# Optimization experiments

Measured on AMD Instinct MI355X. Metric: run time of the kernel, lower is better.

Reference implementation:

```python
import jax, jax.numpy as jnp
import numpy as np

B, L, D = 8, 4096, 1024


def setup_inputs() -> dict:
    key = jax.random.key(0)
    k1, k2, k3 = jax.random.split(key, 3)
    x = jax.random.normal(k1, (B, L, D), dtype=jnp.float32)
    # nn.Linear(d_model, d_model): weight [D, D] (out, in), bias [D]
    bound = 1.0 / np.sqrt(D)
    W = jax.random.uniform(k2, (D, D), dtype=jnp.float32, minval=-bound, maxval=bound)
    b = jax.random.uniform(k3, (D,), dtype=jnp.float32, minval=-bound, maxval=bound)
    return {"x": x, "W": W, "b": b}


def reference(x, W, b):
    # rfft then irfft with n = original length along the sequence dim.
    # (Mathematically the identity on real input, but we keep the ops to
    # match the original module's computation faithfully.)
    x_fft = jnp.fft.rfft(x, axis=1)                 # [B, L//2+1, D] complex64
    x_ifft = jnp.fft.irfft(x_fft, n=x.shape[1], axis=1)  # [B, L, D] float32
    # nn.Linear: y = x @ W^T + b
    return jnp.einsum('bld,ed->ble', x_ifft, W) + b
```

## Files before the change

kernel.cpp:

```cpp
#include <hip/hip_runtime.h>
#include <hip/hip_bf16.h>
#include <stdint.h>


typedef __bf16 bf16_t;
typedef __bf16 bf16x8 __attribute__((ext_vector_type(8)));
typedef float f32x4 __attribute__((ext_vector_type(4)));

typedef __attribute__((address_space(1))) const void gvoid;
typedef __attribute__((address_space(3))) void svoid;

__global__ __launch_bounds__(256) void cvt_f32_bf16_kernel(const float* __restrict__ in,
                                                           bf16_t* __restrict__ out, int n8) {
  int i = blockIdx.x * 256 + threadIdx.x;
  if (i >= n8) return;
  const f32x4* p = (const f32x4*)in + (size_t)i * 2;
  f32x4 v0 = p[0];
  f32x4 v1 = p[1];
  bf16x8 o;
  o[0] = (bf16_t)v0[0]; o[1] = (bf16_t)v0[1]; o[2] = (bf16_t)v0[2]; o[3] = (bf16_t)v0[3];
  o[4] = (bf16_t)v1[0]; o[5] = (bf16_t)v1[1]; o[6] = (bf16_t)v1[2]; o[7] = (bf16_t)v1[3];
  *(bf16x8*)(out + (size_t)i * 8) = o;
}

__global__ __launch_bounds__(256) void gemm_bt_bias_kernel(
    const bf16_t* __restrict__ A, const bf16_t* __restrict__ B,
    const float* __restrict__ bias, float* __restrict__ C,
    int M, int N, int K) {
  __shared__ __align__(16) bf16_t As[128 * 32];
  __shared__ __align__(16) bf16_t Bs[128 * 32];

  int nwg = gridDim.x;
  int bid = blockIdx.x;
  int wg = bid;
  if ((nwg & 7) == 0) {
    int cpx = nwg >> 3;
    wg = (bid & 7) * cpx + (bid >> 3);
  }
  int ntn = N >> 7;
  int tm = wg / ntn;
  int tn = wg % ntn;

  int tid = threadIdx.x;
  int wave = tid >> 6;
  int lane = tid & 63;
  int qr = lane & 15;
  int qg = lane >> 4;
  int wrow = (wave >> 1) << 6;
  int wcol = (wave & 1) << 6;

  const bf16_t* Ag = A + (size_t)(tm * 128 + (tid >> 2)) * K + (tid & 3) * 8;
  const bf16_t* Bg = B + (size_t)(tn * 128 + (tid >> 2)) * K + (tid & 3) * 8;
  bf16_t* Asw = As + tid * 8;
  bf16_t* Bsw = Bs + tid * 8;
  const size_t half = (size_t)64 * K;

  f32x4 acc[4][4] = {};

  for (int k0 = 0; k0 < K; k0 += 32) {
    __builtin_amdgcn_global_load_lds((gvoid*)(Ag + k0), (svoid*)(Asw), 16, 0, 0);
    __builtin_amdgcn_global_load_lds((gvoid*)(Ag + half + k0), (svoid*)(Asw + 2048), 16, 0, 0);
    __builtin_amdgcn_global_load_lds((gvoid*)(Bg + k0), (svoid*)(Bsw), 16, 0, 0);
    __builtin_amdgcn_global_load_lds((gvoid*)(Bg + half + k0), (svoid*)(Bsw + 2048), 16, 0, 0);
    __syncthreads();

    bf16x8 af[4], bfr[4];
#pragma unroll
    for (int m = 0; m < 4; ++m)
      af[m] = *(const bf16x8*)(As + (wrow + m * 16 + qr) * 32 + qg * 8);
#pragma unroll
    for (int n = 0; n < 4; ++n)
      bfr[n] = *(const bf16x8*)(Bs + (wcol + n * 16 + qr) * 32 + qg * 8);
#pragma unroll
    for (int m = 0; m < 4; ++m)
#pragma unroll
      for (int n = 0; n < 4; ++n)
        acc[m][n] = __builtin_amdgcn_mfma_f32_16x16x32_bf16(af[m], bfr[n], acc[m][n], 0, 0, 0);

    __syncthreads();
  }

  int col0 = tn * 128 + wcol;
  float bv[4];
#pragma unroll
  for (int n = 0; n < 4; ++n) bv[n] = bias[col0 + n * 16 + qr];
  size_t rbase = (size_t)(tm * 128 + wrow + qg * 4);
#pragma unroll
  for (int m = 0; m < 4; ++m) {
#pragma unroll
    for (int r = 0; r < 4; ++r) {
      float* crow = C + (rbase + m * 16 + r) * N;
#pragma unroll
      for (int n = 0; n < 4; ++n)
        crow[col0 + n * 16 + qr] = acc[m][n][r] + bv[n];
    }
  }
}

__global__ __launch_bounds__(256) void naive_kernel(const float* __restrict__ x,
                                                    const float* __restrict__ W,
                                                    const float* __restrict__ b,
                                                    float* __restrict__ out,
                                                    int M, int N, int K) {
  long idx = (long)blockIdx.x * 256 + threadIdx.x;
  if (idx >= (long)M * N) return;
  int m = (int)(idx / N), n = (int)(idx % N);
  const float* xr = x + (size_t)m * K;
  const float* wr = W + (size_t)n * K;
  float s = 0.f;
  for (int k = 0; k < K; ++k) s += xr[k] * wr[k];
  out[idx] = s + b[n];
}

extern "C" void kernel_launch(void* const* d_in, const int* in_sizes, int n_in,
                              void* d_out, int out_size, void* d_ws, size_t ws_size,
                              hipStream_t stream) {
  const float* x = (const float*)d_in[0];
  const float* W = (const float*)d_in[1];
  const float* b = (const float*)d_in[2];
  float* out = (float*)d_out;

  int D = in_sizes[2];
  int M = in_sizes[0] / D;
  int N = D, K = D;

  size_t need = (size_t)(4u << 20) + (size_t)M * (size_t)K * sizeof(bf16_t);
  bool fast = (ws_size >= need) && (M % 128 == 0) && (N % 128 == 0) && (K % 32 == 0) &&
              (in_sizes[1] == N * K);

  if (fast) {
    bf16_t* Wb = (bf16_t*)d_ws;
    bf16_t* Xb = (bf16_t*)((char*)d_ws + (4u << 20));
    int n8w = (N * K) / 8;
    hipLaunchKernelGGL(cvt_f32_bf16_kernel, dim3((n8w + 255) / 256), dim3(256), 0, stream,
                       W, Wb, n8w);
    int n8x = (int)(((size_t)M * K) / 8);
    hipLaunchKernelGGL(cvt_f32_bf16_kernel, dim3((n8x + 255) / 256), dim3(256), 0, stream,
                       x, Xb, n8x);
    int nwg = (M / 128) * (N / 128);
    hipLaunchKernelGGL(gemm_bt_bias_kernel, dim3(nwg), dim3(256), 0, stream,
                       Xb, Wb, b, out, M, N, K);
  } else {
    long total = (long)M * N;
    hipLaunchKernelGGL(naive_kernel, dim3((int)((total + 255) / 256)), dim3(256), 0, stream,
                       x, W, b, out, M, N, K);
  }
}
```

Baseline: 141.8 us.

## Use 256x256 tiles, fragment-ordered bf16 layout, and an 8-phase pipelined MFMA GEMM

The conversion kernels now write X and W in an MFMA-fragment-ordered bf16 layout, so each wave's LDS fragment is a contiguous 512-element block. The GEMM moves to 256x256 tiles with 512 threads and a double-buffered 64 KB LDS ring. Loads are issued directly into LDS and interleaved across eight phases per iteration, with vmcnt gating, barriers and raised priority around the MFMA bursts. The goal is to overlap global loads with compute and raise arithmetic intensity, in exchange for more registers and LDS per block, fewer workgroups, and a stricter fast-path condition that K/32 be a power of two.

```diff
diff --git a/kernel.cpp b/kernel.cpp
--- a/kernel.cpp
+++ b/kernel.cpp
@@ -10,91 +10,135 @@
 typedef __attribute__((address_space(1))) const void gvoid;
 typedef __attribute__((address_space(3))) void svoid;
 
-__global__ __launch_bounds__(256) void cvt_f32_bf16_kernel(const float* __restrict__ in,
-                                                           bf16_t* __restrict__ out, int n8) {
-  int i = blockIdx.x * 256 + threadIdx.x;
-  if (i >= n8) return;
-  const f32x4* p = (const f32x4*)in + (size_t)i * 2;
-  f32x4 v0 = p[0];
-  f32x4 v1 = p[1];
+__global__ __launch_bounds__(256) void cvt_frag_kernel(const float* __restrict__ in,
+                                                       bf16_t* __restrict__ out,
+                                                       int K, int ksh, long total8) {
+  long tid = (long)blockIdx.x * 256 + threadIdx.x;
+  if (tid >= total8) return;
+  int lane = (int)(tid & 63);
+  long s = tid >> 6;
+  int kb = (int)(s & ((1 << ksh) - 1));
+  long m16 = s >> ksh;
+  long row = m16 * 16 + (lane & 15);
+  int k0 = kb * 32 + (lane >> 4) * 8;
+  const float* p = in + row * (long)K + k0;
+  f32x4 v0 = *(const f32x4*)p;
+  f32x4 v1 = *(const f32x4*)(p + 4);
   bf16x8 o;
   o[0] = (bf16_t)v0[0]; o[1] = (bf16_t)v0[1]; o[2] = (bf16_t)v0[2]; o[3] = (bf16_t)v0[3];
   o[4] = (bf16_t)v1[0]; o[5] = (bf16_t)v1[1]; o[6] = (bf16_t)v1[2]; o[7] = (bf16_t)v1[3];
-  *(bf16x8*)(out + (size_t)i * 8) = o;
+  *(bf16x8*)(out + tid * 8) = o;
 }
 
-__global__ __launch_bounds__(256) void gemm_bt_bias_kernel(
+
+__device__ __forceinline__ void stage_half(const bf16_t* __restrict__ base, int tile16,
+                                           int kdiv32, int t, int kb, int isB, int buf,
+                                           bf16_t* lds, int wid, int lane8) {
+#pragma unroll
+  for (int r = 0; r < 2; ++r) {
+    int s = r * 8 + wid;
+    size_t gElem = ((((size_t)(tile16 + s)) * kdiv32 + (size_t)(t * 2 + kb)) << 9) + lane8;
+    int dElem = buf * 32768 + isB * 16384 + (s * 2 + kb) * 512 + lane8;
+    __builtin_amdgcn_global_load_lds((gvoid*)(base + gElem), (svoid*)(lds + dElem), 16, 0, 0);
+  }
+}
+
+#define GATE6() asm volatile("s_waitcnt vmcnt(6)" ::: "memory")
+#define BAR() __builtin_amdgcn_s_barrier()
+
+__global__ __launch_bounds__(512, 2) void gemm8p_kernel(
     const bf16_t* __restrict__ A, const bf16_t* __restrict__ B,
     const float* __restrict__ bias, float* __restrict__ C,
     int M, int N, int K) {
-  __shared__ __align__(16) bf16_t As[128 * 32];
-  __shared__ __align__(16) bf16_t Bs[128 * 32];
+  __shared__ __align__(16) bf16_t lds[65536];
+
+  const int kdiv32 = K >> 5;
+  const int NT = K >> 6;
 
   int nwg = gridDim.x;
   int bid = blockIdx.x;
   int wg = bid;
-  if ((nwg & 7) == 0) {
-    int cpx = nwg >> 3;
-    wg = (bid & 7) * cpx + (bid >> 3);
-  }
-  int ntn = N >> 7;
-  int tm = wg / ntn;
-  int tn = wg % ntn;
+  if ((nwg & 7) == 0) wg = (bid & 7) * (nwg >> 3) + (bid >> 3);
+  int ntn = N >> 8;
+  int tm = wg / ntn, tn = wg % ntn;
 
   int tid = threadIdx.x;
-  int wave = tid >> 6;
-  int lane = tid & 63;
-  int qr = lane & 15;
-  int qg = lane >> 4;
-  int wrow = (wave >> 1) << 6;
-  int wcol = (wave & 1) << 6;
+  int wid = tid >> 6, lane = tid & 63;
+  int wm = wid >> 2, wn = wid & 3;
+  int qr = lane & 15, qg = lane >> 4;
+  int lane8 = lane * 8;
+  int wm8 = wm * 8;
+  int wn4 = wn * 4;
+  int tm16 = tm * 16, tn16 = tn * 16;
 
-  const bf16_t* Ag = A + (size_t)(tm * 128 + (tid >> 2)) * K + (tid & 3) * 8;
-  const bf16_t* Bg = B + (size_t)(tn * 128 + (tid >> 2)) * K + (tid & 3) * 8;
-  bf16_t* Asw = As + tid * 8;
-  bf16_t* Bsw = Bs + tid * 8;
-  const size_t half = (size_t)64 * K;
+  f32x4 acc[8][4] = {};
+  bf16x8 aF[8], bF[2];
 
-  f32x4 acc[4][4] = {};
+#define STAGE_A(t, kb, buf) stage_half(A, tm16, kdiv32, (t), (kb), 0, (buf), lds, wid, lane8)
+#define STAGE_B(t, kb, buf) stage_half(B, tn16, kdiv32, (t), (kb), 1, (buf), lds, wid, lane8)
+#define LDA_(mm, kb, buf) (*(const bf16x8*)(lds + (buf)*32768 + ((wm8 + (mm)) * 2 + (kb)) * 512 + lane8))
+#define LDB_(nn, kb, buf) (*(const bf16x8*)(lds + (buf)*32768 + 16384 + ((wn4 + (nn)) * 2 + (kb)) * 512 + lane8))
 
-  for (int k0 = 0; k0 < K; k0 += 32) {
-    __builtin_amdgcn_global_load_lds((gvoid*)(Ag + k0), (svoid*)(Asw), 16, 0, 0);
-    __builtin_amdgcn_global_load_lds((gvoid*)(Ag + half + k0), (svoid*)(Asw + 2048), 16, 0, 0);
-    __builtin_amdgcn_global_load_lds((gvoid*)(Bg + k0), (svoid*)(Bsw), 16, 0, 0);
-    __builtin_amdgcn_global_load_lds((gvoid*)(Bg + half + k0), (svoid*)(Bsw + 2048), 16, 0, 0);
-    __syncthreads();
+#define PHASE(buf, kb, nh, LOADA, STMT_STAGE, DO_GATE)                                     \
+  do {                                                                                     \
+    if (LOADA) {                                                                           \
+      _Pragma("unroll") for (int m_ = 0; m_ < 8; ++m_) aF[m_] = LDA_(m_, kb, buf);         \
+    }                                                                                      \
+    bF[0] = LDB_(2 * (nh) + 0, kb, buf);                                                   \
+    bF[1] = LDB_(2 * (nh) + 1, kb, buf);                                                   \
+    STMT_STAGE;                                                                            \
+    if (DO_GATE) GATE6();                                                                  \
+    BAR();                                                                                 \
+    __builtin_amdgcn_s_setprio(1);                                                         \
+    _Pragma("unroll") for (int m_ = 0; m_ < 8; ++m_) {                                     \
+      acc[m_][2 * (nh) + 0] = __builtin_amdgcn_mfma_f32_16x16x32_bf16(                     \
+          aF[m_], bF[0], acc[m_][2 * (nh) + 0], 0, 0, 0);                                  \
+      acc[m_][2 * (nh) + 1] = __builtin_amdgcn_mfma_f32_16x16x32_bf16(                     \
+          aF[m_], bF[1], acc[m_][2 * (nh) + 1], 0, 0, 0);                                  \
+    }                                                                                      \
+    __builtin_amdgcn_s_setprio(0);                                                         \
+    BAR();                                                                                 \
+  } while (0)
 
-    bf16x8 af[4], bfr[4];
-#pragma unroll
-    for (int m = 0; m < 4; ++m)
-      af[m] = *(const bf16x8*)(As + (wrow + m * 16 + qr) * 32 + qg * 8);
-#pragma unroll
-    for (int n = 0; n < 4; ++n)
-      bfr[n] = *(const bf16x8*)(Bs + (wcol + n * 16 + qr) * 32 + qg * 8);
-#pragma unroll
-    for (int m = 0; m < 4; ++m)
-#pragma unroll
-      for (int n = 0; n < 4; ++n)
-        acc[m][n] = __builtin_amdgcn_mfma_f32_16x16x32_bf16(af[m], bfr[n], acc[m][n], 0, 0, 0);
+  STAGE_A(0, 0, 0); STAGE_B(0, 0, 0); STAGE_A(0, 1, 0); STAGE_B(0, 1, 0);
+  STAGE_A(1, 0, 1); STAGE_B(1, 0, 1); STAGE_A(1, 1, 1);
+  GATE6();
+  BAR();
 
-    __syncthreads();
+  for (int i = 0; i < (NT >> 1); ++i) {
+    int t1 = 2 * i + 1;
+    int t2 = 2 * i + 2; if (t2 >= NT) t2 -= 2;
+    int t3 = 2 * i + 3; if (t3 >= NT) t3 -= 2;
+    PHASE(0, 0, 0, 1, STAGE_B(t1, 1, 1), 0);
+    PHASE(0, 0, 1, 0, STAGE_A(t2, 0, 0), 0);
+    PHASE(0, 1, 0, 1, STAGE_B(t2, 0, 0), 0);
+    PHASE(0, 1, 1, 0, STAGE_A(t2, 1, 0), 1);
+    PHASE(1, 0, 0, 1, STAGE_B(t2, 1, 0), 0);
+    PHASE(1, 0, 1, 0, STAGE_A(t3, 0, 1), 0);
+    PHASE(1, 1, 0, 1, STAGE_B(t3, 0, 1), 0);
+    PHASE(1, 1, 1, 0, STAGE_A(t3, 1, 1), 1);
   }
 
-  int col0 = tn * 128 + wcol;
+  int col0 = tn * 256 + wn * 64;
+  int row0 = tm * 256 + wm * 128;
   float bv[4];
 #pragma unroll
   for (int n = 0; n < 4; ++n) bv[n] = bias[col0 + n * 16 + qr];
-  size_t rbase = (size_t)(tm * 128 + wrow + qg * 4);
 #pragma unroll
-  for (int m = 0; m < 4; ++m) {
+  for (int m = 0; m < 8; ++m) {
 #pragma unroll
     for (int r = 0; r < 4; ++r) {
-      float* crow = C + (rbase + m * 16 + r) * N;
+      float* cr = C + (size_t)(row0 + m * 16 + qg * 4 + r) * N;
 #pragma unroll
       for (int n = 0; n < 4; ++n)
-        crow[col0 + n * 16 + qr] = acc[m][n][r] + bv[n];
+        cr[col0 + n * 16 + qr] = acc[m][n][r] + bv[n];
     }
   }
+#undef PHASE
+#undef STAGE_A
+#undef STAGE_B
+#undef LDA_
+#undef LDB_
 }
 
 __global__ __launch_bounds__(256) void naive_kernel(const float* __restrict__ x,
@@ -124,21 +168,27 @@
   int M = in_sizes[0] / D;
   int N = D, K = D;
 
+  int kdiv32 = K >> 5;
   size_t need = (size_t)(4u << 20) + (size_t)M * (size_t)K * sizeof(bf16_t);
-  bool fast = (ws_size >= need) && (M % 128 == 0) && (N % 128 == 0) && (K % 32 == 0) &&
-              (in_sizes[1] == N * K);
+  bool fast = (ws_size >= need) && (M % 256 == 0) && (N % 256 == 0) && (K % 128 == 0) &&
+              (K >= 128) && ((kdiv32 & (kdiv32 - 1)) == 0) && (in_sizes[1] == N * K);
 
   if (fast) {
+    int ksh = 0;
+    while ((1 << (ksh + 1)) <= kdiv32) ++ksh;
+
     bf16_t* Wb = (bf16_t*)d_ws;
     bf16_t* Xb = (bf16_t*)((char*)d_ws + (4u << 20));
-    int n8w = (N * K) / 8;
-    hipLaunchKernelGGL(cvt_f32_bf16_kernel, dim3((n8w + 255) / 256), dim3(256), 0, stream,
-                       W, Wb, n8w);
-    int n8x = (int)(((size_t)M * K) / 8);
-    hipLaunchKernelGGL(cvt_f32_bf16_kernel, dim3((n8x + 255) / 256), dim3(256), 0, stream,
-                       x, Xb, n8x);
-    int nwg = (M / 128) * (N / 128);
-    hipLaunchKernelGGL(gemm_bt_bias_kernel, dim3(nwg), dim3(256), 0, stream,
+
+    long tW = (long)N * K / 8;
+    hipLaunchKernelGGL(cvt_frag_kernel, dim3((unsigned)((tW + 255) / 256)), dim3(256), 0, stream,
+                       W, Wb, K, ksh, tW);
+    long tX = (long)M * K / 8;
+    hipLaunchKernelGGL(cvt_frag_kernel, dim3((unsigned)((tX + 255) / 256)), dim3(256), 0, stream,
+                       x, Xb, K, ksh, tX);
+
+    int nwg = (M / 256) * (N / 256);
+    hipLaunchKernelGGL(gemm8p_kernel, dim3(nwg), dim3(512), 0, stream,
                        Xb, Wb, b, out, M, N, K);
   } else {
     long total = (long)M * N;
```

Result: faster. 119.0 us (-16.1%).
